# Performance work log

Measured on AMD Instinct MI355X. Metric: run time of the kernel, lower is better.

Reference implementation:

```python
import jax, jax.numpy as jnp
import numpy as np

G, N, E, F_IN, F_OUT, C = 256, 512, 4096, 64, 64, 16


def setup_inputs() -> dict:
    key = jax.random.key(0)
    ks = jax.random.split(key, 6)
    x_batch = jax.random.normal(ks[0], (G, N, F_IN), dtype=jnp.float32)
    edge_index_batch = jax.random.randint(ks[1], (G, 2, E), 0, N, dtype=jnp.int32)
    conv_weight = jax.random.normal(ks[2], (F_OUT, F_IN), dtype=jnp.float32) * (1.0 / np.sqrt(F_IN))
    conv_bias = jax.random.normal(ks[3], (F_OUT,), dtype=jnp.float32) * 0.02
    lin_weight = jax.random.normal(ks[4], (C, F_OUT * N), dtype=jnp.float32) * (1.0 / np.sqrt(F_OUT * N))
    lin_bias = jax.random.normal(ks[5], (C,), dtype=jnp.float32) * 0.02
    return {"x_batch": x_batch, "edge_index_batch": edge_index_batch,
            "conv_weight": conv_weight, "conv_bias": conv_bias,
            "lin_weight": lin_weight, "lin_bias": lin_bias}


def _gcn_conv_graph(xw, edge_index, self_loops):
    # xw: [N, F_OUT] (already linearly transformed), edge_index: [2, E]
    row = jnp.concatenate([edge_index[0], self_loops])  # sources
    col = jnp.concatenate([edge_index[1], self_loops])  # targets
    ones = jnp.ones(row.shape[0], dtype=xw.dtype)
    deg = jax.ops.segment_sum(ones, col, num_segments=N)  # degree at target nodes
    dinv = jnp.where(deg > 0, jax.lax.rsqrt(deg), jnp.zeros_like(deg))
    norm = dinv[row] * dinv[col]                          # [E+N]
    msgs = xw[row] * norm[:, None]                        # gather + normalize
    return jax.ops.segment_sum(msgs, col, num_segments=N)  # scatter-add at targets


def reference(x_batch, edge_index_batch, conv_weight, conv_bias, lin_weight, lin_bias):
    # GCNConv (PyG defaults: self-loops, symmetric normalization, post-agg bias)
    xw = jnp.einsum('gnf,of->gno', x_batch, conv_weight)  # [G, N, F_OUT]
    self_loops = jnp.arange(N, dtype=edge_index_batch.dtype)
    h = jax.vmap(_gcn_conv_graph, in_axes=(0, 0, None))(xw, edge_index_batch, self_loops)
    h = h + conv_bias
    h = jax.nn.relu(h)
    flat = h.reshape(h.shape[0], -1)                      # [G, N*F_OUT]
    logits = flat @ lin_weight.T + lin_bias               # [G, C]
    return jax.nn.log_softmax(logits, axis=-1)
```

## Files before the change

kernel.cpp:

```cpp
#include <hip/hip_runtime.h>

#define Gn 256
#define Nn 512
#define En 4096
#define Fn 64
#define Cn 16
#define ET (En + Nn)

typedef _Float16 halfv8 __attribute__((ext_vector_type(8)));
typedef _Float16 halfv4 __attribute__((ext_vector_type(4)));
typedef float    f32x4  __attribute__((ext_vector_type(4)));

__device__ __forceinline__ float pk_norm(unsigned p) {
    return (float)__builtin_bit_cast(_Float16, (unsigned short)(p & 0xffffu));
}

__global__ __launch_bounds__(1024, 4) void gcn_agg_conv(
    const float* __restrict__ x,
    const int*   __restrict__ ei,
    const float* __restrict__ w,
    const float* __restrict__ wbias,
    _Float16* __restrict__ hout)
{
    __shared__ unsigned short xs_h[Nn * Fn];
    __shared__ unsigned short xhs[Nn * Fn];
    __shared__ unsigned short wts[Fn * Fn];
    __shared__ unsigned int   epk[ET + 8];
    __shared__ float dinv[Nn];
    __shared__ int   cnt[Nn];
    __shared__ int   wsum[8];

    const int g    = blockIdx.x;
    const int tid  = threadIdx.x;
    const int lane = tid & 63;
    const int wid  = tid >> 6;

    const float* xg = x + (size_t)g * Nn * Fn;
    const int*   es = ei + (size_t)g * 2 * En;
    const int*   ed = es + En;

    if (tid < Nn) dinv[tid] = 1.0f;
    __syncthreads();

    for (int e = tid; e < En; e += 1024) atomicAdd(&dinv[ed[e]], 1.0f);
    #pragma unroll
    for (int it = 0; it < 8; ++it) {
        int idx = tid + it * 1024;
        float4 v = *(const float4*)(xg + idx * 4);
        halfv4 hv; hv[0]=(_Float16)v.x; hv[1]=(_Float16)v.y;
                   hv[2]=(_Float16)v.z; hv[3]=(_Float16)v.w;
        *(halfv4*)((char*)xs_h + idx * 8) = hv;
    }
    {
        int o = tid >> 4, f0 = (tid & 15) * 4;
        float4 v = *(const float4*)(w + o * Fn + f0);
        halfv4 hv; hv[0]=(_Float16)v.x; hv[1]=(_Float16)v.y;
                   hv[2]=(_Float16)v.z; hv[3]=(_Float16)v.w;
        int blk = f0 >> 3, hf = (f0 >> 2) & 1;
        *(halfv4*)((char*)wts + o * 128 + ((blk ^ (o & 7)) * 16) + hf * 8) = hv;
    }
    __syncthreads();

    int c = 0;
    if (tid < Nn) { float d = dinv[tid]; c = (int)d; dinv[tid] = rsqrtf(d); }
    int v_ = c;
    #pragma unroll
    for (int off = 1; off < 64; off <<= 1) {
        int u = __shfl_up(v_, off, 64);
        if (lane >= off) v_ += u;
    }
    if (wid < 8 && lane == 63) wsum[wid] = v_;
    __syncthreads();
    if (tid == 0) { int a = 0; for (int i = 0; i < 8; ++i) { int t = wsum[i]; wsum[i] = a; a += t; } }
    __syncthreads();
    if (tid < Nn) cnt[tid] = v_ - c + wsum[wid];
    __syncthreads();

    for (int e = tid; e < ET; e += 1024) {
        int s, t;
        if (e < En) { s = es[e]; t = ed[e]; } else { s = e - En; t = s; }
        float nrm = dinv[s] * dinv[t];
        int slot = atomicAdd(&cnt[t], 1);
        unsigned short nb = __builtin_bit_cast(unsigned short, (_Float16)nrm);
        epk[slot] = ((unsigned)s << 16) | nb;
    }
    __syncthreads();

    {
        const int qid = lane >> 4, fl = lane & 15;
        for (int r = 0; r < 8; ++r) {
            int t = r * 64 + wid * 4 + qid;
            int beg = (t == 0) ? 0 : cnt[t - 1];
            int end = cnt[t];
            float a0 = 0.f, a1 = 0.f, a2 = 0.f, a3 = 0.f;
            unsigned pA0 = epk[beg],     pA1 = epk[beg + 1];
            unsigned pA2 = epk[beg + 2], pA3 = epk[beg + 3];
            int j = beg;
            for (; j + 4 <= end; j += 4) {
                unsigned pB0 = epk[j + 4], pB1 = epk[j + 5];
                unsigned pB2 = epk[j + 6], pB3 = epk[j + 7];
                int s0 = pA0 >> 16, s1 = pA1 >> 16, s2 = pA2 >> 16, s3 = pA3 >> 16;
                float n0 = pk_norm(pA0), n1 = pk_norm(pA1);
                float n2 = pk_norm(pA2), n3 = pk_norm(pA3);
                halfv4 x0 = *(const halfv4*)((const char*)xs_h + s0 * 128 + fl * 8);
                halfv4 x1 = *(const halfv4*)((const char*)xs_h + s1 * 128 + fl * 8);
                halfv4 x2 = *(const halfv4*)((const char*)xs_h + s2 * 128 + fl * 8);
                halfv4 x3 = *(const halfv4*)((const char*)xs_h + s3 * 128 + fl * 8);
                a0 += n0 * (float)x0[0] + n1 * (float)x1[0] + n2 * (float)x2[0] + n3 * (float)x3[0];
                a1 += n0 * (float)x0[1] + n1 * (float)x1[1] + n2 * (float)x2[1] + n3 * (float)x3[1];
                a2 += n0 * (float)x0[2] + n1 * (float)x1[2] + n2 * (float)x2[2] + n3 * (float)x3[2];
                a3 += n0 * (float)x0[3] + n1 * (float)x1[3] + n2 * (float)x2[3] + n3 * (float)x3[3];
                pA0 = pB0; pA1 = pB1; pA2 = pB2; pA3 = pB3;
            }
            for (; j < end; ++j) {
                int s = pA0 >> 16;
                float nm = pk_norm(pA0);
                halfv4 xv = *(const halfv4*)((const char*)xs_h + s * 128 + fl * 8);
                a0 += nm * (float)xv[0]; a1 += nm * (float)xv[1];
                a2 += nm * (float)xv[2]; a3 += nm * (float)xv[3];
                pA0 = pA1; pA1 = pA2; pA2 = pA3;
            }
            halfv4 hv; hv[0]=(_Float16)a0; hv[1]=(_Float16)a1;
                       hv[2]=(_Float16)a2; hv[3]=(_Float16)a3;
            int dw = t * 32 + (((fl >> 1) ^ (t & 7)) * 4) + (fl & 1) * 2;
            *(halfv4*)((char*)xhs + dw * 4) = hv;
        }
    }
    __syncthreads();

    {
        const int m = lane & 15, q = lane >> 4;
        #pragma unroll
        for (int j = 0; j < 8; ++j) {
            int idx = wid * 8 + j, tm = idx >> 2, to = idx & 3;
            int n = tm * 16 + m, o = to * 16 + m;
            halfv8 X0 = *(const halfv8*)((const char*)xhs + n * 128 + ((q       ^ (n & 7)) * 16));
            halfv8 X1 = *(const halfv8*)((const char*)xhs + n * 128 + (((4 + q) ^ (n & 7)) * 16));
            halfv8 W0 = *(const halfv8*)((const char*)wts + o * 128 + ((q       ^ (o & 7)) * 16));
            halfv8 W1 = *(const halfv8*)((const char*)wts + o * 128 + (((4 + q) ^ (o & 7)) * 16));
            f32x4 acc = {0.f, 0.f, 0.f, 0.f};
            acc = __builtin_amdgcn_mfma_f32_16x16x32_f16(W0, X0, acc, 0, 0, 0);
            acc = __builtin_amdgcn_mfma_f32_16x16x32_f16(W1, X1, acc, 0, 0, 0);
            float4 bq = *(const float4*)&wbias[to * 16 + q * 4];
            halfv4 hv;
            hv[0] = (_Float16)fmaxf(acc[0] + bq.x, 0.0f);
            hv[1] = (_Float16)fmaxf(acc[1] + bq.y, 0.0f);
            hv[2] = (_Float16)fmaxf(acc[2] + bq.z, 0.0f);
            hv[3] = (_Float16)fmaxf(acc[3] + bq.w, 0.0f);
            int sw = (to * 4 + q) ^ m;
            *(halfv4*)((char*)xs_h + n * 128 + sw * 8) = hv;
        }
    }
    __syncthreads();

    {
        _Float16* hg = hout + (size_t)g * (Nn * Fn);
        #pragma unroll
        for (int it = 0; it < 8; ++it) {
            int i = tid + it * 1024;
            int n = i >> 4, g64 = i & 15;
            uint2 vv = *(const uint2*)((const char*)xs_h + (n * 16 + (g64 ^ (n & 15))) * 8);
            *(uint2*)((char*)hg + (size_t)i * 8) = vv;
        }
    }
}

__global__ __launch_bounds__(256) void gcn_linear(
    const _Float16* __restrict__ h,
    const float* __restrict__ lw,
    float* __restrict__ part)
{
    __shared__ float red[4][64][4];
    const int cx = blockIdx.x;
    const int gy = blockIdx.y;
    const int tid = threadIdx.x, lane = tid & 63, wid = tid >> 6;
    const int ml = lane & 15, q = lane >> 4;

    const size_t kbase = (size_t)cx * 1024 + wid * 256;
    const _Float16* ha = h  + (size_t)(gy * 16 + ml) * (Nn * Fn) + kbase + q * 8;
    const float*    lb = lw + (size_t)ml * (Nn * Fn) + kbase + q * 8;

    f32x4 acc = {0.f, 0.f, 0.f, 0.f};
    #pragma unroll
    for (int ks = 0; ks < 8; ++ks) {
        halfv8 a = *(const halfv8*)(ha + ks * 32);
        float4 b0 = *(const float4*)(lb + ks * 32);
        float4 b1 = *(const float4*)(lb + ks * 32 + 4);
        halfv8 b; b[0]=(_Float16)b0.x; b[1]=(_Float16)b0.y; b[2]=(_Float16)b0.z;
                  b[3]=(_Float16)b0.w; b[4]=(_Float16)b1.x; b[5]=(_Float16)b1.y;
                  b[6]=(_Float16)b1.z; b[7]=(_Float16)b1.w;
        acc = __builtin_amdgcn_mfma_f32_16x16x32_f16(a, b, acc, 0, 0, 0);
    }
    #pragma unroll
    for (int r = 0; r < 4; ++r) red[wid][lane][r] = acc[r];
    __syncthreads();
    {
        int m = tid >> 4, cc = tid & 15;
        int sl = (m >> 2) * 16 + cc, rg = m & 3;
        float v = red[0][sl][rg] + red[1][sl][rg] + red[2][sl][rg] + red[3][sl][rg];
        part[(((size_t)(gy * 16 + m)) * 32 + cx) * Cn + cc] = v;
    }
}

__global__ __launch_bounds__(64) void gcn_softmax(
    const float* __restrict__ part,
    const float* __restrict__ lbias,
    float* __restrict__ out)
{
    const int g = blockIdx.x, lane = threadIdx.x;
    if (lane < Cn) {
        float v = lbias[lane];
        #pragma unroll
        for (int s = 0; s < 32; ++s) v += part[((size_t)g * 32 + s) * Cn + lane];
        float m = v;
        #pragma unroll
        for (int off = 8; off > 0; off >>= 1) m = fmaxf(m, __shfl_xor(m, off, 16));
        float ex = expf(v - m);
        float ssum = ex;
        #pragma unroll
        for (int off = 8; off > 0; off >>= 1) ssum += __shfl_xor(ssum, off, 16);
        out[g * Cn + lane] = v - m - logf(ssum);
    }
}

extern "C" void kernel_launch(void* const* d_in, const int* in_sizes, int n_in,
                              void* d_out, int out_size, void* d_ws, size_t ws_size,
                              hipStream_t stream) {
    const float* x  = (const float*)d_in[0];
    const int*   ei = (const int*)d_in[1];
    const float* w  = (const float*)d_in[2];
    const float* wb = (const float*)d_in[3];
    const float* lw = (const float*)d_in[4];
    const float* lb = (const float*)d_in[5];
    float* out = (float*)d_out;

    _Float16* hbuf = (_Float16*)d_ws;
    float* part = (float*)((char*)d_ws + (size_t)Gn * Nn * Fn * 2);

    hipLaunchKernelGGL(gcn_agg_conv, dim3(Gn), dim3(1024), 0, stream,
                       x, ei, w, wb, hbuf);
    hipLaunchKernelGGL(gcn_linear, dim3(32, 16), dim3(256), 0, stream,
                       hbuf, lw, part);
    hipLaunchKernelGGL(gcn_softmax, dim3(Gn), dim3(64), 0, stream,
                       part, lb, out);
}
```

Baseline: 113.4 us.

## Fuse linear layer and log-softmax into GCN conv kernel with fp16 weights

After: 130.8 us. 1.15x slower.

```diff
diff --git a/kernel.cpp b/kernel.cpp
--- a/kernel.cpp
+++ b/kernel.cpp
@@ -9,18 +9,55 @@
 
 typedef _Float16 halfv8 __attribute__((ext_vector_type(8)));
 typedef _Float16 halfv4 __attribute__((ext_vector_type(4)));
+typedef _Float16 halfv2 __attribute__((ext_vector_type(2)));
 typedef float    f32x4  __attribute__((ext_vector_type(4)));
 
 __device__ __forceinline__ float pk_norm(unsigned p) {
     return (float)__builtin_bit_cast(_Float16, (unsigned short)(p & 0xffffu));
 }
 
-__global__ __launch_bounds__(1024, 4) void gcn_agg_conv(
+#if __has_builtin(__builtin_amdgcn_fdot2)
+__device__ __forceinline__ float fdot2_(halfv2 a, halfv2 b, float c) {
+    return __builtin_amdgcn_fdot2(a, b, c, false);
+}
+#else
+__device__ __forceinline__ float fdot2_(halfv2 a, halfv2 b, float c) {
+    return c + (float)a[0] * (float)b[0] + (float)a[1] * (float)b[1];
+}
+#endif
+
+struct H2x4 { halfv2 p0, p1, p2, p3; };
+
+__device__ __forceinline__ float dot8(halfv8 l, halfv8 h, float c) {
+    H2x4 L = __builtin_bit_cast(H2x4, l);
+    H2x4 H = __builtin_bit_cast(H2x4, h);
+    c = fdot2_(L.p0, H.p0, c);
+    c = fdot2_(L.p1, H.p1, c);
+    c = fdot2_(L.p2, H.p2, c);
+    c = fdot2_(L.p3, H.p3, c);
+    return c;
+}
+
+__global__ __launch_bounds__(256) void cvt_lw(const float* __restrict__ lw,
+                                              _Float16* __restrict__ lwh) {
+    int i = (blockIdx.x * 256 + threadIdx.x) * 2;
+    #pragma unroll
+    for (int r = 0; r < 2; ++r) {
+        float4 v = *(const float4*)(lw + (size_t)(i + r) * 4);
+        halfv4 h; h[0]=(_Float16)v.x; h[1]=(_Float16)v.y;
+                  h[2]=(_Float16)v.z; h[3]=(_Float16)v.w;
+        *(halfv4*)((char*)lwh + (size_t)(i + r) * 8) = h;
+    }
+}
+
+__global__ __launch_bounds__(1024, 4) void gcn_fused(
     const float* __restrict__ x,
     const int*   __restrict__ ei,
     const float* __restrict__ w,
     const float* __restrict__ wbias,
-    _Float16* __restrict__ hout)
+    const _Float16* __restrict__ lwh,
+    const float* __restrict__ lbias,
+    float* __restrict__ out)
 {
     __shared__ unsigned short xs_h[Nn * Fn];
     __shared__ unsigned short xhs[Nn * Fn];
@@ -147,79 +184,68 @@
             hv[1] = (_Float16)fmaxf(acc[1] + bq.y, 0.0f);
             hv[2] = (_Float16)fmaxf(acc[2] + bq.z, 0.0f);
             hv[3] = (_Float16)fmaxf(acc[3] + bq.w, 0.0f);
-            int sw = (to * 4 + q) ^ m;
-            *(halfv4*)((char*)xs_h + n * 128 + sw * 8) = hv;
-        }
-    }
-    __syncthreads();
-
-    {
-        _Float16* hg = hout + (size_t)g * (Nn * Fn);
+            *(halfv4*)((char*)xs_h + n * 128 + (to * 16 + q * 4) * 2) = hv;
+        }
+    }
+    __syncthreads();
+
+    {
+        const int k0 = tid * 32;
+        halfv8 hr0 = *(const halfv8*)((const char*)xs_h + k0 * 2);
+        halfv8 hr1 = *(const halfv8*)((const char*)xs_h + k0 * 2 + 16);
+        halfv8 hr2 = *(const halfv8*)((const char*)xs_h + k0 * 2 + 32);
+        halfv8 hr3 = *(const halfv8*)((const char*)xs_h + k0 * 2 + 48);
+
+        float* wredf = dinv;
         #pragma unroll
-        for (int it = 0; it < 8; ++it) {
-            int i = tid + it * 1024;
-            int n = i >> 4, g64 = i & 15;
-            uint2 vv = *(const uint2*)((const char*)xs_h + (n * 16 + (g64 ^ (n & 15))) * 8);
-            *(uint2*)((char*)hg + (size_t)i * 8) = vv;
-        }
-    }
-}
-
-__global__ __launch_bounds__(256) void gcn_linear(
-    const _Float16* __restrict__ h,
-    const float* __restrict__ lw,
-    float* __restrict__ part)
-{
-    __shared__ float red[4][64][4];
-    const int cx = blockIdx.x;
-    const int gy = blockIdx.y;
-    const int tid = threadIdx.x, lane = tid & 63, wid = tid >> 6;
-    const int ml = lane & 15, q = lane >> 4;
-
-    const size_t kbase = (size_t)cx * 1024 + wid * 256;
-    const _Float16* ha = h  + (size_t)(gy * 16 + ml) * (Nn * Fn) + kbase + q * 8;
-    const float*    lb = lw + (size_t)ml * (Nn * Fn) + kbase + q * 8;
-
-    f32x4 acc = {0.f, 0.f, 0.f, 0.f};
-    #pragma unroll
-    for (int ks = 0; ks < 8; ++ks) {
-        halfv8 a = *(const halfv8*)(ha + ks * 32);
-        float4 b0 = *(const float4*)(lb + ks * 32);
-        float4 b1 = *(const float4*)(lb + ks * 32 + 4);
-        halfv8 b; b[0]=(_Float16)b0.x; b[1]=(_Float16)b0.y; b[2]=(_Float16)b0.z;
-                  b[3]=(_Float16)b0.w; b[4]=(_Float16)b1.x; b[5]=(_Float16)b1.y;
-                  b[6]=(_Float16)b1.z; b[7]=(_Float16)b1.w;
-        acc = __builtin_amdgcn_mfma_f32_16x16x32_f16(a, b, acc, 0, 0, 0);
-    }
-    #pragma unroll
-    for (int r = 0; r < 4; ++r) red[wid][lane][r] = acc[r];
-    __syncthreads();
-    {
-        int m = tid >> 4, cc = tid & 15;
-        int sl = (m >> 2) * 16 + cc, rg = m & 3;
-        float v = red[0][sl][rg] + red[1][sl][rg] + red[2][sl][rg] + red[3][sl][rg];
-        part[(((size_t)(gy * 16 + m)) * 32 + cx) * Cn + cc] = v;
-    }
-}
-
-__global__ __launch_bounds__(64) void gcn_softmax(
-    const float* __restrict__ part,
-    const float* __restrict__ lbias,
-    float* __restrict__ out)
-{
-    const int g = blockIdx.x, lane = threadIdx.x;
-    if (lane < Cn) {
-        float v = lbias[lane];
-        #pragma unroll
-        for (int s = 0; s < 32; ++s) v += part[((size_t)g * 32 + s) * Cn + lane];
-        float m = v;
-        #pragma unroll
-        for (int off = 8; off > 0; off >>= 1) m = fmaxf(m, __shfl_xor(m, off, 16));
-        float ex = expf(v - m);
-        float ssum = ex;
-        #pragma unroll
-        for (int off = 8; off > 0; off >>= 1) ssum += __shfl_xor(ssum, off, 16);
-        out[g * Cn + lane] = v - m - logf(ssum);
+        for (int cb = 0; cb < 4; ++cb) {
+            const halfv8* lp0 = (const halfv8*)(lwh + (size_t)(cb*4+0) * (Nn*Fn) + k0);
+            const halfv8* lp1 = (const halfv8*)(lwh + (size_t)(cb*4+1) * (Nn*Fn) + k0);
+            const halfv8* lp2 = (const halfv8*)(lwh + (size_t)(cb*4+2) * (Nn*Fn) + k0);
+            const halfv8* lp3 = (const halfv8*)(lwh + (size_t)(cb*4+3) * (Nn*Fn) + k0);
+            halfv8 l00=lp0[0], l01=lp0[1], l02=lp0[2], l03=lp0[3];
+            halfv8 l10=lp1[0], l11=lp1[1], l12=lp1[2], l13=lp1[3];
+            halfv8 l20=lp2[0], l21=lp2[1], l22=lp2[2], l23=lp2[3];
+            halfv8 l30=lp3[0], l31=lp3[1], l32=lp3[2], l33=lp3[3];
+            float a0 = 0.f, a1 = 0.f, a2 = 0.f, a3 = 0.f;
+            a0 = dot8(l00, hr0, a0); a1 = dot8(l10, hr0, a1);
+            a2 = dot8(l20, hr0, a2); a3 = dot8(l30, hr0, a3);
+            a0 = dot8(l01, hr1, a0); a1 = dot8(l11, hr1, a1);
+            a2 = dot8(l21, hr1, a2); a3 = dot8(l31, hr1, a3);
+            a0 = dot8(l02, hr2, a0); a1 = dot8(l12, hr2, a1);
+            a2 = dot8(l22, hr2, a2); a3 = dot8(l32, hr2, a3);
+            a0 = dot8(l03, hr3, a0); a1 = dot8(l13, hr3, a1);
+            a2 = dot8(l23, hr3, a2); a3 = dot8(l33, hr3, a3);
+
+            #pragma unroll
+            for (int off = 32; off > 0; off >>= 1) {
+                a0 += __shfl_down(a0, off, 64);
+                a1 += __shfl_down(a1, off, 64);
+                a2 += __shfl_down(a2, off, 64);
+                a3 += __shfl_down(a3, off, 64);
+            }
+            if (lane == 0) {
+                wredf[wid * 16 + cb * 4 + 0] = a0;
+                wredf[wid * 16 + cb * 4 + 1] = a1;
+                wredf[wid * 16 + cb * 4 + 2] = a2;
+                wredf[wid * 16 + cb * 4 + 3] = a3;
+            }
+        }
+        __syncthreads();
+
+        if (wid == 0 && lane < Cn) {
+            float v = lbias[lane];
+            #pragma unroll
+            for (int k = 0; k < 16; ++k) v += wredf[k * 16 + lane];
+            float m = v;
+            #pragma unroll
+            for (int off = 8; off > 0; off >>= 1) m = fmaxf(m, __shfl_xor(m, off, 16));
+            float ex = expf(v - m);
+            float ssum = ex;
+            #pragma unroll
+            for (int off = 8; off > 0; off >>= 1) ssum += __shfl_xor(ssum, off, 16);
+            out[g * Cn + lane] = v - m - logf(ssum);
+        }
     }
 }
 
@@ -234,13 +260,9 @@
     const float* lb = (const float*)d_in[5];
     float* out = (float*)d_out;
 
-    _Float16* hbuf = (_Float16*)d_ws;
-    float* part = (float*)((char*)d_ws + (size_t)Gn * Nn * Fn * 2);
-
-    hipLaunchKernelGGL(gcn_agg_conv, dim3(Gn), dim3(1024), 0, stream,
-                       x, ei, w, wb, hbuf);
-    hipLaunchKernelGGL(gcn_linear, dim3(32, 16), dim3(256), 0, stream,
-                       hbuf, lw, part);
-    hipLaunchKernelGGL(gcn_softmax, dim3(Gn), dim3(64), 0, stream,
-                       part, lb, out);
-}
+    _Float16* lwh = (_Float16*)d_ws;
+
+    hipLaunchKernelGGL(cvt_lw, dim3(Gn), dim3(256), 0, stream, lw, lwh);
+    hipLaunchKernelGGL(gcn_fused, dim3(Gn), dim3(1024), 0, stream,
+                       x, ei, w, wb, lwh, lb, out);
+}
```
